# Kernel tuning notes

Measured on AMD Instinct MI355X. Metric: run time of the kernel, lower is better.

## Reference

```python
import jax, jax.numpy as jnp
import numpy as np

EMBED_DIM = 1024
NUM_HEADS = 16
HEAD_DIM = EMBED_DIM // NUM_HEADS
ROPE_BASE = 10000.0


def _rope_angles(seq_len, head_dim):
    inv_freq = 1.0 / (ROPE_BASE ** (jnp.arange(0, head_dim, 2, dtype=jnp.float32) / head_dim))  # [D/2]
    pos = jnp.arange(seq_len, dtype=jnp.float32)
    ang = pos[:, None] * inv_freq[None, :]  # [S, D/2]
    return jnp.cos(ang), jnp.sin(ang)


def _apply_rope(t, cos, sin):
    # t: [B, H, S, D]; rotate-half convention
    d2 = t.shape[-1] // 2
    t1, t2 = t[..., :d2], t[..., d2:]
    return jnp.concatenate([t1 * cos - t2 * sin, t2 * cos + t1 * sin], axis=-1)


def setup_inputs() -> dict:
    key = jax.random.key(0)
    ks = jax.random.split(key, 6)
    B, S, E = 1, 4096, EMBED_DIM
    x = jax.random.normal(ks[0], (B, S, E), dtype=jnp.float32)
    # causal mask: True means masked-out (upper triangle above diagonal)
    mask = jnp.triu(jnp.ones((S, S), dtype=bool), k=1)[None, None, :, :]
    scale = 0.02
    wqkv_w = jax.random.normal(ks[1], (E, 3 * E), dtype=jnp.float32) * scale
    wqkv_b = jax.random.normal(ks[2], (3 * E,), dtype=jnp.float32) * scale
    out_w = jax.random.normal(ks[3], (E, E), dtype=jnp.float32) * scale
    out_b = jax.random.normal(ks[4], (E,), dtype=jnp.float32) * scale
    return {"x": x, "mask": mask, "wqkv_w": wqkv_w, "wqkv_b": wqkv_b, "out_w": out_w, "out_b": out_b}


def reference(x, mask, wqkv_w, wqkv_b, out_w, out_b):
    B, S, E = x.shape
    H, D = NUM_HEADS, HEAD_DIM
    qkv = x @ wqkv_w + wqkv_b  # [B, S, 3E]
    q, k, v = jnp.split(qkv, 3, axis=-1)
    # [B, S, E] -> [B, H, S, D]
    q = q.reshape(B, S, H, D).transpose(0, 2, 1, 3)
    k = k.reshape(B, S, H, D).transpose(0, 2, 1, 3)
    v = v.reshape(B, S, H, D).transpose(0, 2, 1, 3)
    cos, sin = _rope_angles(S, D)  # [S, D/2]
    q = _apply_rope(q, cos, sin)
    k = _apply_rope(k, cos, sin)
    scores = jnp.einsum('bhqd,bhkd->bhqk', q, k) * (D ** -0.5)  # [B, H, S, S]
    scores = jnp.where(mask[:, :, -S:, :], -jnp.inf, scores)
    weights = jax.nn.softmax(scores, axis=-1)
    ctx = jnp.einsum('bhqk,bhkd->bhqd', weights, v)  # [B, H, S, D]
    ctx = ctx.transpose(0, 2, 1, 3).reshape(B, S, E)
    return ctx @ out_w + out_b
```

## Files before the change

kernel.cpp:

```cpp
#include <hip/hip_runtime.h>
#include <hip/hip_bf16.h>
#include <math.h>

#define S_LEN 4096
#define EMB   1024
#define E3    3072
#define NH    16
#define HD    64

typedef unsigned short u16;
typedef short          bfrag __attribute__((ext_vector_type(8)));
typedef float          ffrag __attribute__((ext_vector_type(4)));
typedef unsigned short us8   __attribute__((ext_vector_type(8)));
typedef unsigned short us4   __attribute__((ext_vector_type(4)));

__device__ __forceinline__ u16 f2bf(float f) {
    union { float f; unsigned u; } v; v.f = f;
    unsigned r = v.u + 0x7fffu + ((v.u >> 16) & 1u);
    return (u16)(r >> 16);
}
__device__ __forceinline__ unsigned pack_bf16_trunc(float lo, float hi) {
    union { float f; unsigned u; } a, b; a.f = lo; b.f = hi;
    return __builtin_amdgcn_perm(b.u, a.u, 0x07060302u);
}
__device__ __forceinline__ void gld16(const void* g, void* l) {
    __builtin_amdgcn_global_load_lds(
        (const __attribute__((address_space(1))) unsigned int*)g,
        (__attribute__((address_space(3))) unsigned int*)l, 16, 0, 0);
}

__global__ __launch_bounds__(256)
void cast_bf16_kernel(const float* __restrict__ in, u16* __restrict__ out) {
    const size_t i = ((size_t)blockIdx.x * 256 + threadIdx.x) * 8;
    float4 a = *(const float4*)(in + i);
    float4 b = *(const float4*)(in + i + 4);
    us8 o;
    o[0]=f2bf(a.x); o[1]=f2bf(a.y); o[2]=f2bf(a.z); o[3]=f2bf(a.w);
    o[4]=f2bf(b.x); o[5]=f2bf(b.y); o[6]=f2bf(b.z); o[7]=f2bf(b.w);
    *(us8*)(out + i) = o;
}

__global__ __launch_bounds__(256)
void transpose_cast_kernel(const float* __restrict__ in, u16* __restrict__ out,
                           int R, int C) {
    __shared__ u16 T[64][72];
    const int r0 = blockIdx.x * 64, c0 = blockIdx.y * 64;
    const int t = threadIdx.x;
    const int rr = t >> 2, cc = (t & 3) * 16;

    const float* ip = in + (size_t)(r0 + rr) * C + c0 + cc;
    u16 tmp[16];
    #pragma unroll
    for (int i4 = 0; i4 < 4; i4++) {
        float4 v = ((const float4*)ip)[i4];
        tmp[4*i4+0]=f2bf(v.x); tmp[4*i4+1]=f2bf(v.y);
        tmp[4*i4+2]=f2bf(v.z); tmp[4*i4+3]=f2bf(v.w);
    }
    #pragma unroll
    for (int i8 = 0; i8 < 2; i8++) {
        us8 vv;
        #pragma unroll
        for (int j = 0; j < 8; j++) vv[j] = tmp[8*i8+j];
        *(us8*)&T[rr][cc + 8*i8] = vv;
    }
    __syncthreads();

    const int oc = t >> 2, orr = (t & 3) * 16;
    u16 ot[16];
    #pragma unroll
    for (int j = 0; j < 16; j++) ot[j] = T[orr + j][oc];
    u16* op = out + (size_t)(c0 + oc) * R + r0 + orr;
    #pragma unroll
    for (int i8 = 0; i8 < 2; i8++) {
        us8 vv;
        #pragma unroll
        for (int j = 0; j < 8; j++) vv[j] = ot[8*i8+j];
        *(us8*)(op + 8*i8) = vv;
    }
}

template <int OUT_BF16, int NT, int ROPE, int MINW>
__global__ __launch_bounds__(256, MINW)
void gemm_bt_kernel(const u16* __restrict__ A, const u16* __restrict__ Bt,
                    const float* __restrict__ bias, void* __restrict__ Cv,
                    u16* __restrict__ vtp, int M, int N, int K) {
    constexpr int BN = 32 * NT;
    constexpr int WS = 16 * NT;
    __shared__ u16 As[2][128][32];
    __shared__ u16 Bs[2][BN][32];

    const int tid = threadIdx.x;
    const int w = tid >> 6, L = tid & 63;
    const int col = L & 15, quad = L >> 4;
    const int wm = w & 1, wn = w >> 1;
    const int m0 = blockIdx.x * 128, n0 = blockIdx.y * BN;

    ffrag acc[4][NT];
    #pragma unroll
    for (int a = 0; a < 4; a++)
        #pragma unroll
        for (int b = 0; b < NT; b++)
            #pragma unroll
            for (int r = 0; r < 4; r++) acc[a][b][r] = 0.f;

    const int srow = L >> 2;
    const int schk = L & 3;

    #pragma unroll
    for (int t = 0; t < 2; t++) {
        const int rg = (2 * w + t) * 16;
        gld16(A + (size_t)(m0 + rg + srow) * K + schk * 8, &As[0][rg][0]);
    }
    #pragma unroll
    for (int t = 0; t < NT / 2; t++) {
        const int rg = (w * (NT / 2) + t) * 16;
        gld16(Bt + (size_t)(n0 + rg + srow) * K + schk * 8, &Bs[0][rg][0]);
    }
    __syncthreads();

    int buf = 0;
    for (int k0 = 0; k0 < K; k0 += 32, buf ^= 1) {
        if (k0 + 32 < K) {
            #pragma unroll
            for (int t = 0; t < 2; t++) {
                const int rg = (2 * w + t) * 16;
                gld16(A + (size_t)(m0 + rg + srow) * K + k0 + 32 + schk * 8,
                      &As[buf ^ 1][rg][0]);
            }
            #pragma unroll
            for (int t = 0; t < NT / 2; t++) {
                const int rg = (w * (NT / 2) + t) * 16;
                gld16(Bt + (size_t)(n0 + rg + srow) * K + k0 + 32 + schk * 8,
                      &Bs[buf ^ 1][rg][0]);
            }
        }

        bfrag af[4], bf[NT];
        #pragma unroll
        for (int mt = 0; mt < 4; mt++)
            af[mt] = *(const bfrag*)&As[buf][64 * wm + 16 * mt + col][8 * quad];
        #pragma unroll
        for (int nt = 0; nt < NT; nt++)
            bf[nt] = *(const bfrag*)&Bs[buf][WS * wn + 16 * nt + col][8 * quad];
        #pragma unroll
        for (int mt = 0; mt < 4; mt++)
            #pragma unroll
            for (int nt = 0; nt < NT; nt++)
                acc[mt][nt] = __builtin_amdgcn_mfma_f32_16x16x32_bf16(
                    af[mt], bf[nt], acc[mt][nt], 0, 0, 0);

        __syncthreads();
    }

    float bv[NT];
    #pragma unroll
    for (int nt = 0; nt < NT; nt++) bv[nt] = bias[n0 + WS * wn + 16 * nt + col];

    if (ROPE && n0 < 2 * EMB) {
        const float SCq = (n0 < EMB) ? 0.125f * 1.44269504088896f : 1.0f;
        const float C = 13.287712379549449f / 32.0f;
        float invf[2];
        invf[0] = exp2f(-(float)col * C);
        invf[1] = exp2f(-(float)(col + 16) * C);
        #pragma unroll
        for (int mt = 0; mt < 4; mt++) {
            #pragma unroll
            for (int r = 0; r < 4; r++) {
                const int mrow = m0 + 64 * wm + 16 * mt + 4 * quad + r;
                const float fs = (float)mrow;
                u16* cp = (u16*)Cv + (size_t)mrow * N + n0 + 64 * wn + col;
                #pragma unroll
                for (int pr = 0; pr < 2; pr++) {
                    float sn, cs;
                    sincosf(fs * invf[pr], &sn, &cs);
                    const float t1 = acc[mt][pr][r] + bv[pr];
                    const float t2 = acc[mt][pr + 2][r] + bv[pr + 2];
                    cp[16 * pr]      = f2bf((t1 * cs - t2 * sn) * SCq);
                    cp[16 * pr + 32] = f2bf((t2 * cs + t1 * sn) * SCq);
                }
            }
        }
    } else if (ROPE) {
        #pragma unroll
        for (int nt = 0; nt < NT; nt++) {
            const int dg = n0 - 2 * EMB + WS * wn + 16 * nt + col;
            #pragma unroll
            for (int mt = 0; mt < 4; mt++) {
                const int s0 = m0 + 64 * wm + 16 * mt + 4 * quad;
                us4 pk;
                #pragma unroll
                for (int r = 0; r < 4; r++) pk[r] = f2bf(acc[mt][nt][r] + bv[nt]);
                *(us4*)&vtp[(size_t)dg * S_LEN + s0] = pk;
            }
        }
    } else {
        #pragma unroll
        for (int mt = 0; mt < 4; mt++) {
            #pragma unroll
            for (int r = 0; r < 4; r++) {
                const int m = m0 + 64 * wm + 16 * mt + 4 * quad + r;
                #pragma unroll
                for (int nt = 0; nt < NT; nt++) {
                    const int n = n0 + WS * wn + 16 * nt + col;
                    const float val = acc[mt][nt][r] + bv[nt];
                    if (OUT_BF16) ((u16*)Cv)[(size_t)m * N + n] = f2bf(val);
                    else          ((float*)Cv)[(size_t)m * N + n] = val;
                }
            }
        }
    }
}

__global__ __launch_bounds__(128, 2)
void flash7_kernel(const u16* __restrict__ qkvb, const u16* __restrict__ vt,
                   u16* __restrict__ ctxb) {
    __shared__ u16 QP[2][32][64];
    __shared__ u16 Ks[2][64][64];
    __shared__ u16 Vs[2][64][64];

    const int id = blockIdx.x;
    const int h  = (id & 7) | (((id >> 3) & 1) << 3);
    const int a  = (id >> 4) & 15;
    const int b  = id >> 8;
    int qi;
    if      (b == 0) qi = 2 * a;
    else if (b == 1) qi = 63 - 2 * a;
    else if (b == 2) qi = 2 * a + 1;
    else             qi = 62 - 2 * a;
    const int q0 = qi * 64;
    const int ntk = qi + 1;

    const int tid = threadIdx.x;
    const int w = tid >> 6, L = tid & 63;
    const int col = L & 15, quad = L >> 4;
    const int lr = L >> 3, lp = L & 7;
    const int lc = lp ^ lr;

    const size_t kArow = (size_t)(32 * w + lr) * E3 + EMB + h * HD + lc * 8;
    const size_t vArow = ((size_t)h * HD + 32 * w + lr) * S_LEN + lc * 8;

    #pragma unroll
    for (int u = 0; u < 4; u++) {
        gld16(qkvb + (size_t)(q0 + 32 * w + 8 * u + lr) * E3 + h * HD + lc * 8,
              &QP[w][8 * u][0]);
        gld16(qkvb + kArow + (size_t)(8 * u) * E3, &Ks[0][32 * w + 8 * u][0]);
        gld16(vt + vArow + (size_t)(8 * u) * S_LEN, &Vs[0][32 * w + 8 * u][0]);
    }
    __syncthreads();

    bfrag qf[2][2];
    #pragma unroll
    for (int i = 0; i < 2; i++)
        #pragma unroll
        for (int ks = 0; ks < 2; ks++)
            qf[i][ks] = *(const bfrag*)
                ((const char*)&QP[w][16 * i + col][0] +
                 16 * ((4 * ks + quad) ^ (col & 7)));

    bfrag ones;
    #pragma unroll
    for (int i = 0; i < 8; i++) ones[i] = (short)0x3F80;

    ffrag o[4][2], ol[2];
    #pragma unroll
    for (int d4 = 0; d4 < 4; d4++)
        #pragma unroll
        for (int i = 0; i < 2; i++)
            #pragma unroll
            for (int r = 0; r < 4; r++) o[d4][i][r] = 0.f;
    #pragma unroll
    for (int i = 0; i < 2; i++)
        #pragma unroll
        for (int r = 0; r < 4; r++) ol[i][r] = 0.f;

    #pragma unroll 1
    for (int t = 0; t < ntk; t++) {
        const int buf = t & 1;
        if (t + 1 < ntk) {
            const size_t ko = kArow + (size_t)(t + 1) * 64 * E3;
            const size_t vo = vArow + (size_t)(t + 1) * 64;
            #pragma unroll
            for (int u = 0; u < 4; u++) {
                gld16(qkvb + ko + (size_t)(8 * u) * E3,
                      &Ks[buf ^ 1][32 * w + 8 * u][0]);
                gld16(vt + vo + (size_t)(8 * u) * S_LEN,
                      &Vs[buf ^ 1][32 * w + 8 * u][0]);
            }
        }

        ffrag st[4][2];
        #pragma unroll
        for (int t4 = 0; t4 < 4; t4++)
            #pragma unroll
            for (int i = 0; i < 2; i++)
                #pragma unroll
                for (int r = 0; r < 4; r++) st[t4][i][r] = 0.f;
        #pragma unroll
        for (int ks = 0; ks < 2; ks++) {
            bfrag kf[4];
            #pragma unroll
            for (int t4 = 0; t4 < 4; t4++)
                kf[t4] = *(const bfrag*)
                    &Ks[buf][16 * t4 + col][(((4 * ks + quad) ^ (col & 7)) * 8)];
            #pragma unroll
            for (int t4 = 0; t4 < 4; t4++)
                #pragma unroll
                for (int i = 0; i < 2; i++)
                    st[t4][i] = __builtin_amdgcn_mfma_f32_16x16x32_bf16(
                        kf[t4], qf[i][ks], st[t4][i], 0, 0, 0);
        }

        if (t == ntk - 1) {
            #pragma unroll
            for (int i = 0; i < 2; i++) {
                const int qrel = 32 * w + 16 * i + col;
                #pragma unroll
                for (int t4 = 0; t4 < 4; t4++) {
                    const int key0 = 16 * t4 + 4 * quad;
                    #pragma unroll
                    for (int r = 0; r < 4; r++)
                        if (key0 + r > qrel) st[t4][i][r] = -3.0e38f;
                }
            }
        }

        #pragma unroll
        for (int i = 0; i < 2; i++) {
            const int prow = 16 * i + col;
            #pragma unroll
            for (int t4 = 0; t4 < 4; t4++) {
                float pr[4];
                #pragma unroll
                for (int r = 0; r < 4; r++) pr[r] = exp2f(st[t4][i][r]);
                uint2 pk;
                pk.x = pack_bf16_trunc(pr[0], pr[1]);
                pk.y = pack_bf16_trunc(pr[2], pr[3]);
                const int c2 = (2 * t4 + (quad >> 1)) ^ (col & 7);
                *(uint2*)((char*)&QP[w][prow][0] + 16 * c2 + 8 * (quad & 1)) = pk;
            }
        }

        #pragma unroll
        for (int ks = 0; ks < 2; ks++) {
            bfrag vf[4];
            #pragma unroll
            for (int d4 = 0; d4 < 4; d4++)
                vf[d4] = *(const bfrag*)
                    &Vs[buf][16 * d4 + col][(((4 * ks + quad) ^ (col & 7)) * 8)];
            bfrag pf[2];
            #pragma unroll
            for (int i = 0; i < 2; i++)
                pf[i] = *(const bfrag*)
                    ((const char*)&QP[w][16 * i + col][0] +
                     16 * ((4 * ks + quad) ^ (col & 7)));
            #pragma unroll
            for (int d4 = 0; d4 < 4; d4++)
                #pragma unroll
                for (int i = 0; i < 2; i++)
                    o[d4][i] = __builtin_amdgcn_mfma_f32_16x16x32_bf16(
                        vf[d4], pf[i], o[d4][i], 0, 0, 0);
            #pragma unroll
            for (int i = 0; i < 2; i++)
                ol[i] = __builtin_amdgcn_mfma_f32_16x16x32_bf16(
                    ones, pf[i], ol[i], 0, 0, 0);
        }

        __syncthreads();
    }

    #pragma unroll
    for (int i = 0; i < 2; i++) {
        const float inv = 1.0f / ol[i][0];
        const int qg = q0 + 32 * w + 16 * i + col;
        #pragma unroll
        for (int d4 = 0; d4 < 4; d4++) {
            us4 pk;
            #pragma unroll
            for (int r = 0; r < 4; r++) pk[r] = f2bf(o[d4][i][r] * inv);
            *(us4*)&ctxb[(size_t)qg * EMB + h * HD + 16 * d4 + 4 * quad] = pk;
        }
    }
}

extern "C" void kernel_launch(void* const* d_in, const int* in_sizes, int n_in,
                              void* d_out, int out_size, void* d_ws, size_t ws_size,
                              hipStream_t stream) {
    const float* x      = (const float*)d_in[0];
    const float* wqkv_w = (const float*)d_in[2];
    const float* wqkv_b = (const float*)d_in[3];
    const float* out_w  = (const float*)d_in[4];
    const float* out_b  = (const float*)d_in[5];
    float* out = (float*)d_out;

    u16* qkvb = (u16*)d_ws;
    u16* ctxb = qkvb + (size_t)S_LEN * E3;
    u16* xb   = ctxb + (size_t)S_LEN * EMB;
    u16* wt   = xb   + (size_t)S_LEN * EMB;
    u16* owt  = wt   + (size_t)E3 * EMB;
    u16* vtb  = owt  + (size_t)EMB * EMB;

    dim3 blk(256);

    cast_bf16_kernel<<<dim3(S_LEN * EMB / (256 * 8)), blk, 0, stream>>>(x, xb);
    transpose_cast_kernel<<<dim3(EMB / 64, E3 / 64), blk, 0, stream>>>(
        wqkv_w, wt, EMB, E3);
    transpose_cast_kernel<<<dim3(EMB / 64, EMB / 64), blk, 0, stream>>>(
        out_w, owt, EMB, EMB);

    gemm_bt_kernel<1, 4, 1, 3><<<dim3(S_LEN / 128, E3 / 128), blk, 0, stream>>>(
        xb, wt, wqkv_b, qkvb, vtb, S_LEN, E3, EMB);

    flash7_kernel<<<dim3(1024), dim3(128), 0, stream>>>(qkvb, vtb, ctxb);

    gemm_bt_kernel<0, 2, 0, 2><<<dim3(S_LEN / 128, EMB / 64), blk, 0, stream>>>(
        ctxb, owt, out_b, out, nullptr, S_LEN, EMB, EMB);
}
```

Before: 269.8 us.

## Split attention keys across warps with direct global K/V loads and LDS combine

The flash kernel now gives each block 32 query rows instead of 64 and launches twice as many blocks. The two warps share the same queries but each takes half of every 64-key tile, and the partial outputs and row sums are combined through shared memory at the end. K and V fragments are loaded straight from global memory into registers, so the shared-memory staging, double buffering and per-tile barriers are gone. This trades LDS reuse and prefetch overlap for more parallelism and higher occupancy, at the cost of more uncoalesced global traffic and exposed load latency.

```diff
diff --git a/kernel.cpp b/kernel.cpp
--- a/kernel.cpp
+++ b/kernel.cpp
@@ -211,42 +211,26 @@
     }
 }
 
-__global__ __launch_bounds__(128, 2)
-void flash7_kernel(const u16* __restrict__ qkvb, const u16* __restrict__ vt,
+__global__ __launch_bounds__(128, 4)
+void flash8_kernel(const u16* __restrict__ qkvb, const u16* __restrict__ vt,
                    u16* __restrict__ ctxb) {
-    __shared__ u16 QP[2][32][64];
-    __shared__ u16 Ks[2][64][64];
-    __shared__ u16 Vs[2][64][64];
+    __shared__ u16 Ps[2][32][32];
+    __shared__ float comb[34 * 64];
 
     const int id = blockIdx.x;
-    const int h  = (id & 7) | (((id >> 3) & 1) << 3);
-    const int a  = (id >> 4) & 15;
-    const int b  = id >> 8;
-    int qi;
-    if      (b == 0) qi = 2 * a;
-    else if (b == 1) qi = 63 - 2 * a;
-    else if (b == 2) qi = 2 * a + 1;
-    else             qi = 62 - 2 * a;
-    const int q0 = qi * 64;
-    const int ntk = qi + 1;
+    const int h  = id & 15;
+    const int qq = id >> 4;
+    const int rr = qq >> 4, aa = qq & 15;
+    const int qi = (rr & 1) ? ((rr >> 1) * 32 + 31 - aa) : ((rr >> 1) * 32 + aa);
+    const int q0 = qi * 32;
+    const int ntk = qi / 2 + 1;
 
     const int tid = threadIdx.x;
     const int w = tid >> 6, L = tid & 63;
     const int col = L & 15, quad = L >> 4;
-    const int lr = L >> 3, lp = L & 7;
-    const int lc = lp ^ lr;
-
-    const size_t kArow = (size_t)(32 * w + lr) * E3 + EMB + h * HD + lc * 8;
-    const size_t vArow = ((size_t)h * HD + 32 * w + lr) * S_LEN + lc * 8;
-
-    #pragma unroll
-    for (int u = 0; u < 4; u++) {
-        gld16(qkvb + (size_t)(q0 + 32 * w + 8 * u + lr) * E3 + h * HD + lc * 8,
-              &QP[w][8 * u][0]);
-        gld16(qkvb + kArow + (size_t)(8 * u) * E3, &Ks[0][32 * w + 8 * u][0]);
-        gld16(vt + vArow + (size_t)(8 * u) * S_LEN, &Vs[0][32 * w + 8 * u][0]);
-    }
-    __syncthreads();
+
+    int nwt = ntk;
+    if (((qi & 1) == 0) && w == 1) nwt--;
 
     bfrag qf[2][2];
     #pragma unroll
@@ -254,8 +238,7 @@
         #pragma unroll
         for (int ks = 0; ks < 2; ks++)
             qf[i][ks] = *(const bfrag*)
-                ((const char*)&QP[w][16 * i + col][0] +
-                 16 * ((4 * ks + quad) ^ (col & 7)));
+                (qkvb + (size_t)(q0 + 16 * i + col) * E3 + h * HD + 32 * ks + 8 * quad);
 
     bfrag ones;
     #pragma unroll
@@ -273,49 +256,51 @@
         #pragma unroll
         for (int r = 0; r < 4; r++) ol[i][r] = 0.f;
 
+    const u16* kp0 = qkvb + (size_t)(32 * w + col) * E3 + EMB + h * HD + 8 * quad;
+    const u16* kp1 = kp0 + (size_t)16 * E3;
+    const u16* vp  = vt + ((size_t)h * HD + col) * S_LEN + 32 * w + 8 * quad;
+
+    char* const prow_base = (char*)&Ps[w][0][0];
+
     #pragma unroll 1
-    for (int t = 0; t < ntk; t++) {
-        const int buf = t & 1;
-        if (t + 1 < ntk) {
-            const size_t ko = kArow + (size_t)(t + 1) * 64 * E3;
-            const size_t vo = vArow + (size_t)(t + 1) * 64;
-            #pragma unroll
-            for (int u = 0; u < 4; u++) {
-                gld16(qkvb + ko + (size_t)(8 * u) * E3,
-                      &Ks[buf ^ 1][32 * w + 8 * u][0]);
-                gld16(vt + vo + (size_t)(8 * u) * S_LEN,
-                      &Vs[buf ^ 1][32 * w + 8 * u][0]);
-            }
-        }
-
-        ffrag st[4][2];
-        #pragma unroll
-        for (int t4 = 0; t4 < 4; t4++)
+    for (int t = 0; t < nwt; t++) {
+        const size_t koff = (size_t)t * 64 * E3;
+        const int    voff = t * 64;
+
+        bfrag kf[2][2];
+        #pragma unroll
+        for (int ks = 0; ks < 2; ks++) {
+            kf[0][ks] = *(const bfrag*)(kp0 + koff + 32 * ks);
+            kf[1][ks] = *(const bfrag*)(kp1 + koff + 32 * ks);
+        }
+        bfrag vf[4];
+        #pragma unroll
+        for (int d4 = 0; d4 < 4; d4++)
+            vf[d4] = *(const bfrag*)(vp + (size_t)(16 * d4) * S_LEN + voff);
+
+        ffrag st[2][2];
+        #pragma unroll
+        for (int t4 = 0; t4 < 2; t4++)
             #pragma unroll
             for (int i = 0; i < 2; i++)
                 #pragma unroll
                 for (int r = 0; r < 4; r++) st[t4][i][r] = 0.f;
         #pragma unroll
-        for (int ks = 0; ks < 2; ks++) {
-            bfrag kf[4];
-            #pragma unroll
-            for (int t4 = 0; t4 < 4; t4++)
-                kf[t4] = *(const bfrag*)
-                    &Ks[buf][16 * t4 + col][(((4 * ks + quad) ^ (col & 7)) * 8)];
-            #pragma unroll
-            for (int t4 = 0; t4 < 4; t4++)
+        for (int ks = 0; ks < 2; ks++)
+            #pragma unroll
+            for (int t4 = 0; t4 < 2; t4++)
                 #pragma unroll
                 for (int i = 0; i < 2; i++)
                     st[t4][i] = __builtin_amdgcn_mfma_f32_16x16x32_bf16(
-                        kf[t4], qf[i][ks], st[t4][i], 0, 0, 0);
-        }
+                        kf[t4][ks], qf[i][ks], st[t4][i], 0, 0, 0);
 
         if (t == ntk - 1) {
+            const int kb = 64 * t + 32 * w;
             #pragma unroll
             for (int i = 0; i < 2; i++) {
-                const int qrel = 32 * w + 16 * i + col;
-                #pragma unroll
-                for (int t4 = 0; t4 < 4; t4++) {
+                const int qrel = q0 + 16 * i + col - kb;
+                #pragma unroll
+                for (int t4 = 0; t4 < 2; t4++) {
                     const int key0 = 16 * t4 + 4 * quad;
                     #pragma unroll
                     for (int r = 0; r < 4; r++)
@@ -326,58 +311,66 @@
 
         #pragma unroll
         for (int i = 0; i < 2; i++) {
-            const int prow = 16 * i + col;
-            #pragma unroll
-            for (int t4 = 0; t4 < 4; t4++) {
+            char* const pr_b = prow_base + (16 * i + col) * 64;
+            #pragma unroll
+            for (int t4 = 0; t4 < 2; t4++) {
                 float pr[4];
                 #pragma unroll
                 for (int r = 0; r < 4; r++) pr[r] = exp2f(st[t4][i][r]);
                 uint2 pk;
                 pk.x = pack_bf16_trunc(pr[0], pr[1]);
                 pk.y = pack_bf16_trunc(pr[2], pr[3]);
-                const int c2 = (2 * t4 + (quad >> 1)) ^ (col & 7);
-                *(uint2*)((char*)&QP[w][prow][0] + 16 * c2 + 8 * (quad & 1)) = pk;
-            }
-        }
-
-        #pragma unroll
-        for (int ks = 0; ks < 2; ks++) {
-            bfrag vf[4];
-            #pragma unroll
-            for (int d4 = 0; d4 < 4; d4++)
-                vf[d4] = *(const bfrag*)
-                    &Vs[buf][16 * d4 + col][(((4 * ks + quad) ^ (col & 7)) * 8)];
-            bfrag pf[2];
+                const int c2 = (2 * t4 + (quad >> 1)) ^ (col & 3);
+                *(uint2*)(pr_b + 16 * c2 + 8 * (quad & 1)) = pk;
+            }
+        }
+
+        bfrag pf[2];
+        #pragma unroll
+        for (int i = 0; i < 2; i++)
+            pf[i] = *(const bfrag*)
+                (prow_base + (16 * i + col) * 64 + 16 * (quad ^ (col & 3)));
+        #pragma unroll
+        for (int d4 = 0; d4 < 4; d4++)
             #pragma unroll
             for (int i = 0; i < 2; i++)
-                pf[i] = *(const bfrag*)
-                    ((const char*)&QP[w][16 * i + col][0] +
-                     16 * ((4 * ks + quad) ^ (col & 7)));
-            #pragma unroll
-            for (int d4 = 0; d4 < 4; d4++)
-                #pragma unroll
-                for (int i = 0; i < 2; i++)
-                    o[d4][i] = __builtin_amdgcn_mfma_f32_16x16x32_bf16(
-                        vf[d4], pf[i], o[d4][i], 0, 0, 0);
+                o[d4][i] = __builtin_amdgcn_mfma_f32_16x16x32_bf16(
+                    vf[d4], pf[i], o[d4][i], 0, 0, 0);
+        #pragma unroll
+        for (int i = 0; i < 2; i++)
+            ol[i] = __builtin_amdgcn_mfma_f32_16x16x32_bf16(
+                ones, pf[i], ol[i], 0, 0, 0);
+    }
+
+    if (w == 1) {
+        #pragma unroll
+        for (int d4 = 0; d4 < 4; d4++)
             #pragma unroll
             for (int i = 0; i < 2; i++)
-                ol[i] = __builtin_amdgcn_mfma_f32_16x16x32_bf16(
-                    ones, pf[i], ol[i], 0, 0, 0);
-        }
-
-        __syncthreads();
-    }
-
-    #pragma unroll
-    for (int i = 0; i < 2; i++) {
-        const float inv = 1.0f / ol[i][0];
-        const int qg = q0 + 32 * w + 16 * i + col;
-        #pragma unroll
-        for (int d4 = 0; d4 < 4; d4++) {
-            us4 pk;
-            #pragma unroll
-            for (int r = 0; r < 4; r++) pk[r] = f2bf(o[d4][i][r] * inv);
-            *(us4*)&ctxb[(size_t)qg * EMB + h * HD + 16 * d4 + 4 * quad] = pk;
+                #pragma unroll
+                for (int r = 0; r < 4; r++)
+                    comb[(d4 * 8 + i * 4 + r) * 64 + L] = o[d4][i][r];
+        #pragma unroll
+        for (int i = 0; i < 2; i++)
+            comb[(32 + i) * 64 + L] = ol[i][0];
+    }
+    __syncthreads();
+    if (w == 0) {
+        #pragma unroll
+        for (int i = 0; i < 2; i++) {
+            const float l = ol[i][0] + comb[(32 + i) * 64 + L];
+            const float inv = 1.0f / l;
+            const int qg = q0 + 16 * i + col;
+            #pragma unroll
+            for (int d4 = 0; d4 < 4; d4++) {
+                us4 pk;
+                #pragma unroll
+                for (int r = 0; r < 4; r++) {
+                    const float val = o[d4][i][r] + comb[(d4 * 8 + i * 4 + r) * 64 + L];
+                    pk[r] = f2bf(val * inv);
+                }
+                *(us4*)&ctxb[(size_t)qg * EMB + h * HD + 16 * d4 + 4 * quad] = pk;
+            }
         }
     }
 }
@@ -410,7 +403,7 @@
     gemm_bt_kernel<1, 4, 1, 3><<<dim3(S_LEN / 128, E3 / 128), blk, 0, stream>>>(
         xb, wt, wqkv_b, qkvb, vtb, S_LEN, E3, EMB);
 
-    flash7_kernel<<<dim3(1024), dim3(128), 0, stream>>>(qkvb, vtb, ctxb);
+    flash8_kernel<<<dim3(2048), dim3(128), 0, stream>>>(qkvb, vtb, ctxb);
 
     gemm_bt_kernel<0, 2, 0, 2><<<dim3(S_LEN / 128, EMB / 64), blk, 0, stream>>>(
         ctxb, owt, out_b, out, nullptr, S_LEN, EMB, EMB);
```

New measurement: 301.1 us. 11.6% more time.

## Split long causal query tiles across two blocks and merge partials

Applied to the files above, without the earlier changes.

The attention kernel now uses 256-thread blocks over 128-row query tiles. The upper-half query tiles (the longest causal rows) are split across two blocks that each process half the key range, with bf16 partial outputs and fp32 row sums written to reused workspace. A new combine kernel adds the two partials and normalizes them. This aims to balance work across blocks and raise occupancy, at the cost of an extra launch, extra global traffic, and bf16 rounding of the unnormalized partials.

```diff
diff --git a/kernel.cpp b/kernel.cpp
--- a/kernel.cpp
+++ b/kernel.cpp
@@ -18,6 +18,10 @@
     union { float f; unsigned u; } v; v.f = f;
     unsigned r = v.u + 0x7fffu + ((v.u >> 16) & 1u);
     return (u16)(r >> 16);
+}
+__device__ __forceinline__ float bf2f(u16 b) {
+    union { unsigned u; float f; } v; v.u = ((unsigned)b) << 16;
+    return v.f;
 }
 __device__ __forceinline__ unsigned pack_bf16_trunc(float lo, float hi) {
     union { float f; unsigned u; } a, b; a.f = lo; b.f = hi;
@@ -211,24 +215,25 @@
     }
 }
 
-__global__ __launch_bounds__(128, 2)
-void flash7_kernel(const u16* __restrict__ qkvb, const u16* __restrict__ vt,
-                   u16* __restrict__ ctxb) {
-    __shared__ u16 QP[2][32][64];
+__global__ __launch_bounds__(256, 3)
+void flash9_kernel(const u16* __restrict__ qkvb, const u16* __restrict__ vt,
+                   u16* __restrict__ ctxb, u16* __restrict__ pO,
+                   float* __restrict__ pL) {
+    __shared__ u16 QP[4][32][64];
     __shared__ u16 Ks[2][64][64];
     __shared__ u16 Vs[2][64][64];
 
     const int id = blockIdx.x;
-    const int h  = (id & 7) | (((id >> 3) & 1) << 3);
-    const int a  = (id >> 4) & 15;
-    const int b  = id >> 8;
-    int qi;
-    if      (b == 0) qi = 2 * a;
-    else if (b == 1) qi = 63 - 2 * a;
-    else if (b == 2) qi = 2 * a + 1;
-    else             qi = 62 - 2 * a;
-    const int q0 = qi * 64;
-    const int ntk = qi + 1;
+    const int x  = id & 7;
+    const int r  = id >> 3;
+    const int h  = x + 8 * (r >= 48);
+    const int rr = (r >= 48) ? (r - 48) : r;
+
+    int type, qi, kt0, cnt;
+    if (rr < 16)      { type = 1; qi = 31 - rr;        kt0 = 0;      cnt = qi + 1; }
+    else if (rr < 32) { type = 2; qi = 31 - (rr - 16); kt0 = qi + 1; cnt = qi + 1; }
+    else              { type = 0; qi = 15 - (rr - 32); kt0 = 0;      cnt = 2 * qi + 2; }
+    const int q0 = qi * 128;
 
     const int tid = threadIdx.x;
     const int w = tid >> 6, L = tid & 63;
@@ -236,15 +241,24 @@
     const int lr = L >> 3, lp = L & 7;
     const int lc = lp ^ lr;
 
-    const size_t kArow = (size_t)(32 * w + lr) * E3 + EMB + h * HD + lc * 8;
-    const size_t vArow = ((size_t)h * HD + 32 * w + lr) * S_LEN + lc * 8;
-
-    #pragma unroll
-    for (int u = 0; u < 4; u++) {
+    const bool domask = (type != 1);
+    const int nwt = cnt - ((domask && w < 2) ? 1 : 0);
+
+    const size_t kArow = (size_t)(16 * w + lr) * E3 + EMB + h * HD + lc * 8;
+    const size_t vArow = ((size_t)h * HD + 16 * w + lr) * S_LEN + lc * 8;
+    const size_t kt0off  = (size_t)kt0 * 64 * E3;
+    const size_t vt0off  = (size_t)kt0 * 64;
+
+    #pragma unroll
+    for (int u = 0; u < 4; u++)
         gld16(qkvb + (size_t)(q0 + 32 * w + 8 * u + lr) * E3 + h * HD + lc * 8,
               &QP[w][8 * u][0]);
-        gld16(qkvb + kArow + (size_t)(8 * u) * E3, &Ks[0][32 * w + 8 * u][0]);
-        gld16(vt + vArow + (size_t)(8 * u) * S_LEN, &Vs[0][32 * w + 8 * u][0]);
+    #pragma unroll
+    for (int u = 0; u < 2; u++) {
+        gld16(qkvb + kArow + kt0off + (size_t)(8 * u) * E3,
+              &Ks[0][16 * w + 8 * u][0]);
+        gld16(vt + vArow + vt0off + (size_t)(8 * u) * S_LEN,
+              &Vs[0][16 * w + 8 * u][0]);
     }
     __syncthreads();
 
@@ -267,118 +281,167 @@
         #pragma unroll
         for (int i = 0; i < 2; i++)
             #pragma unroll
-            for (int r = 0; r < 4; r++) o[d4][i][r] = 0.f;
+            for (int r2 = 0; r2 < 4; r2++) o[d4][i][r2] = 0.f;
     #pragma unroll
     for (int i = 0; i < 2; i++)
         #pragma unroll
-        for (int r = 0; r < 4; r++) ol[i][r] = 0.f;
+        for (int r2 = 0; r2 < 4; r2++) ol[i][r2] = 0.f;
 
     #pragma unroll 1
-    for (int t = 0; t < ntk; t++) {
+    for (int t = 0; t < cnt; t++) {
         const int buf = t & 1;
-        if (t + 1 < ntk) {
-            const size_t ko = kArow + (size_t)(t + 1) * 64 * E3;
-            const size_t vo = vArow + (size_t)(t + 1) * 64;
-            #pragma unroll
-            for (int u = 0; u < 4; u++) {
+        if (t + 1 < cnt) {
+            const size_t ko = kArow + kt0off + (size_t)(t + 1) * 64 * E3;
+            const size_t vo = vArow + vt0off + (size_t)(t + 1) * 64;
+            #pragma unroll
+            for (int u = 0; u < 2; u++) {
                 gld16(qkvb + ko + (size_t)(8 * u) * E3,
-                      &Ks[buf ^ 1][32 * w + 8 * u][0]);
+                      &Ks[buf ^ 1][16 * w + 8 * u][0]);
                 gld16(vt + vo + (size_t)(8 * u) * S_LEN,
-                      &Vs[buf ^ 1][32 * w + 8 * u][0]);
-            }
-        }
-
-        ffrag st[4][2];
-        #pragma unroll
-        for (int t4 = 0; t4 < 4; t4++)
-            #pragma unroll
-            for (int i = 0; i < 2; i++)
-                #pragma unroll
-                for (int r = 0; r < 4; r++) st[t4][i][r] = 0.f;
-        #pragma unroll
-        for (int ks = 0; ks < 2; ks++) {
-            bfrag kf[4];
+                      &Vs[buf ^ 1][16 * w + 8 * u][0]);
+            }
+        }
+
+        if (t < nwt) {
+            ffrag st[4][2];
             #pragma unroll
             for (int t4 = 0; t4 < 4; t4++)
-                kf[t4] = *(const bfrag*)
-                    &Ks[buf][16 * t4 + col][(((4 * ks + quad) ^ (col & 7)) * 8)];
-            #pragma unroll
-            for (int t4 = 0; t4 < 4; t4++)
                 #pragma unroll
                 for (int i = 0; i < 2; i++)
-                    st[t4][i] = __builtin_amdgcn_mfma_f32_16x16x32_bf16(
-                        kf[t4], qf[i][ks], st[t4][i], 0, 0, 0);
-        }
-
-        if (t == ntk - 1) {
+                    #pragma unroll
+                    for (int r2 = 0; r2 < 4; r2++) st[t4][i][r2] = 0.f;
+            #pragma unroll
+            for (int ks = 0; ks < 2; ks++) {
+                bfrag kf[4];
+                #pragma unroll
+                for (int t4 = 0; t4 < 4; t4++)
+                    kf[t4] = *(const bfrag*)
+                        &Ks[buf][16 * t4 + col][(((4 * ks + quad) ^ (col & 7)) * 8)];
+                #pragma unroll
+                for (int t4 = 0; t4 < 4; t4++)
+                    #pragma unroll
+                    for (int i = 0; i < 2; i++)
+                        st[t4][i] = __builtin_amdgcn_mfma_f32_16x16x32_bf16(
+                            kf[t4], qf[i][ks], st[t4][i], 0, 0, 0);
+            }
+
+            if (domask && t == nwt - 1) {
+                #pragma unroll
+                for (int i = 0; i < 2; i++) {
+                    const int qrel = 32 * (w & 1) + 16 * i + col;
+                    #pragma unroll
+                    for (int t4 = 0; t4 < 4; t4++) {
+                        const int key0 = 16 * t4 + 4 * quad;
+                        #pragma unroll
+                        for (int r2 = 0; r2 < 4; r2++)
+                            if (key0 + r2 > qrel) st[t4][i][r2] = -3.0e38f;
+                    }
+                }
+            }
+
             #pragma unroll
             for (int i = 0; i < 2; i++) {
-                const int qrel = 32 * w + 16 * i + col;
+                const int prow = 16 * i + col;
                 #pragma unroll
                 for (int t4 = 0; t4 < 4; t4++) {
-                    const int key0 = 16 * t4 + 4 * quad;
+                    float pr[4];
                     #pragma unroll
-                    for (int r = 0; r < 4; r++)
-                        if (key0 + r > qrel) st[t4][i][r] = -3.0e38f;
+                    for (int r2 = 0; r2 < 4; r2++) pr[r2] = exp2f(st[t4][i][r2]);
+                    uint2 pk;
+                    pk.x = pack_bf16_trunc(pr[0], pr[1]);
+                    pk.y = pack_bf16_trunc(pr[2], pr[3]);
+                    const int c2 = (2 * t4 + (quad >> 1)) ^ (col & 7);
+                    *(uint2*)((char*)&QP[w][prow][0] + 16 * c2 + 8 * (quad & 1)) = pk;
                 }
             }
-        }
-
+
+            #pragma unroll
+            for (int ks = 0; ks < 2; ks++) {
+                bfrag vf[4];
+                #pragma unroll
+                for (int d4 = 0; d4 < 4; d4++)
+                    vf[d4] = *(const bfrag*)
+                        &Vs[buf][16 * d4 + col][(((4 * ks + quad) ^ (col & 7)) * 8)];
+                bfrag pf[2];
+                #pragma unroll
+                for (int i = 0; i < 2; i++)
+                    pf[i] = *(const bfrag*)
+                        ((const char*)&QP[w][16 * i + col][0] +
+                         16 * ((4 * ks + quad) ^ (col & 7)));
+                #pragma unroll
+                for (int d4 = 0; d4 < 4; d4++)
+                    #pragma unroll
+                    for (int i = 0; i < 2; i++)
+                        o[d4][i] = __builtin_amdgcn_mfma_f32_16x16x32_bf16(
+                            vf[d4], pf[i], o[d4][i], 0, 0, 0);
+                #pragma unroll
+                for (int i = 0; i < 2; i++)
+                    ol[i] = __builtin_amdgcn_mfma_f32_16x16x32_bf16(
+                        ones, pf[i], ol[i], 0, 0, 0);
+            }
+        }
+
+        __syncthreads();
+    }
+
+    if (type == 0) {
         #pragma unroll
         for (int i = 0; i < 2; i++) {
-            const int prow = 16 * i + col;
-            #pragma unroll
-            for (int t4 = 0; t4 < 4; t4++) {
-                float pr[4];
-                #pragma unroll
-                for (int r = 0; r < 4; r++) pr[r] = exp2f(st[t4][i][r]);
-                uint2 pk;
-                pk.x = pack_bf16_trunc(pr[0], pr[1]);
-                pk.y = pack_bf16_trunc(pr[2], pr[3]);
-                const int c2 = (2 * t4 + (quad >> 1)) ^ (col & 7);
-                *(uint2*)((char*)&QP[w][prow][0] + 16 * c2 + 8 * (quad & 1)) = pk;
-            }
-        }
-
-        #pragma unroll
-        for (int ks = 0; ks < 2; ks++) {
-            bfrag vf[4];
-            #pragma unroll
-            for (int d4 = 0; d4 < 4; d4++)
-                vf[d4] = *(const bfrag*)
-                    &Vs[buf][16 * d4 + col][(((4 * ks + quad) ^ (col & 7)) * 8)];
-            bfrag pf[2];
-            #pragma unroll
-            for (int i = 0; i < 2; i++)
-                pf[i] = *(const bfrag*)
-                    ((const char*)&QP[w][16 * i + col][0] +
-                     16 * ((4 * ks + quad) ^ (col & 7)));
-            #pragma unroll
-            for (int d4 = 0; d4 < 4; d4++)
-                #pragma unroll
-                for (int i = 0; i < 2; i++)
-                    o[d4][i] = __builtin_amdgcn_mfma_f32_16x16x32_bf16(
-                        vf[d4], pf[i], o[d4][i], 0, 0, 0);
-            #pragma unroll
-            for (int i = 0; i < 2; i++)
-                ol[i] = __builtin_amdgcn_mfma_f32_16x16x32_bf16(
-                    ones, pf[i], ol[i], 0, 0, 0);
-        }
-
-        __syncthreads();
-    }
-
-    #pragma unroll
-    for (int i = 0; i < 2; i++) {
-        const float inv = 1.0f / ol[i][0];
-        const int qg = q0 + 32 * w + 16 * i + col;
-        #pragma unroll
-        for (int d4 = 0; d4 < 4; d4++) {
-            us4 pk;
-            #pragma unroll
-            for (int r = 0; r < 4; r++) pk[r] = f2bf(o[d4][i][r] * inv);
-            *(us4*)&ctxb[(size_t)qg * EMB + h * HD + 16 * d4 + 4 * quad] = pk;
-        }
+            const float inv = 1.0f / ol[i][0];
+            const int qg = q0 + 32 * w + 16 * i + col;
+            #pragma unroll
+            for (int d4 = 0; d4 < 4; d4++) {
+                us4 pk;
+                #pragma unroll
+                for (int r2 = 0; r2 < 4; r2++) pk[r2] = f2bf(o[d4][i][r2] * inv);
+                *(us4*)&ctxb[(size_t)qg * EMB + h * HD + 16 * d4 + 4 * quad] = pk;
+            }
+        }
+    } else {
+        const int half = type - 1;
+        const int g = h * 16 + (qi - 16);
+        u16* po = pO + (size_t)half * 256 * 128 * 64 + (size_t)g * 128 * 64;
+        float* pl = pL + half * 256 * 128 + g * 128;
+        #pragma unroll
+        for (int i = 0; i < 2; i++) {
+            const int qrow = 32 * w + 16 * i + col;
+            #pragma unroll
+            for (int d4 = 0; d4 < 4; d4++) {
+                us4 pk;
+                #pragma unroll
+                for (int r2 = 0; r2 < 4; r2++) pk[r2] = f2bf(o[d4][i][r2]);
+                *(us4*)&po[(size_t)qrow * 64 + 16 * d4 + 4 * quad] = pk;
+            }
+            if (quad == 0) pl[qrow] = ol[i][0];
+        }
+    }
+}
+
+__global__ __launch_bounds__(256)
+void combine_kernel(const u16* __restrict__ pO, const float* __restrict__ pL,
+                    u16* __restrict__ ctxb) {
+    const int g = blockIdx.x;
+    const int h = g >> 4, qi = 16 + (g & 15);
+    const int t = threadIdx.x;
+    const int q = t >> 1, dh = (t & 1) * 32;
+
+    const float la = pL[g * 128 + q];
+    const float lb = pL[256 * 128 + g * 128 + q];
+    const float inv = 1.0f / (la + lb);
+
+    const u16* a = pO + ((size_t)g * 128 + q) * 64 + dh;
+    const u16* b = a + (size_t)256 * 128 * 64;
+    u16* op = ctxb + (size_t)(qi * 128 + q) * EMB + h * HD + dh;
+
+    #pragma unroll
+    for (int j = 0; j < 4; j++) {
+        us8 va = *(const us8*)(a + 8 * j);
+        us8 vb = *(const us8*)(b + 8 * j);
+        us8 vo;
+        #pragma unroll
+        for (int e = 0; e < 8; e++)
+            vo[e] = f2bf((bf2f(va[e]) + bf2f(vb[e])) * inv);
+        *(us8*)(op + 8 * j) = vo;
     }
 }
 
@@ -399,6 +462,9 @@
     u16* owt  = wt   + (size_t)E3 * EMB;
     u16* vtb  = owt  + (size_t)EMB * EMB;
 
+    u16*   pO = xb;
+    float* pL = (float*)wt;
+
     dim3 blk(256);
 
     cast_bf16_kernel<<<dim3(S_LEN * EMB / (256 * 8)), blk, 0, stream>>>(x, xb);
@@ -410,7 +476,8 @@
     gemm_bt_kernel<1, 4, 1, 3><<<dim3(S_LEN / 128, E3 / 128), blk, 0, stream>>>(
         xb, wt, wqkv_b, qkvb, vtb, S_LEN, E3, EMB);
 
-    flash7_kernel<<<dim3(1024), dim3(128), 0, stream>>>(qkvb, vtb, ctxb);
+    flash9_kernel<<<dim3(768), blk, 0, stream>>>(qkvb, vtb, ctxb, pO, pL);
+    combine_kernel<<<dim3(256), blk, 0, stream>>>(pO, pL, ctxb);
 
     gemm_bt_kernel<0, 2, 0, 2><<<dim3(S_LEN / 128, EMB / 64), blk, 0, stream>>>(
         ctxb, owt, out_b, out, nullptr, S_LEN, EMB, EMB);
```

Result: faster. 256.3 us (-5.0%).
